# Kernel optimization log

Hardware: AMD Instinct MI355X
Metric: run time of the kernel (lower is better)

The kernel has to match this reference:

```python
import jax, jax.numpy as jnp
import numpy as np

B, T, ENC_H, DEC_H, P = 64, 2048, 512, 512, 256


def setup_inputs() -> dict:
    key = jax.random.key(0)
    ks = jax.random.split(key, 9)
    s_enc = 1.0 / np.sqrt(ENC_H)
    s_dec = 1.0 / np.sqrt(DEC_H)
    return {
        "decoder_output_embedding": jax.random.normal(ks[0], (B, DEC_H), jnp.float32),
        "encoder_outputs": jax.random.normal(ks[1], (B, T, ENC_H), jnp.float32),
        "encoder_lens": jax.random.randint(ks[2], (B,), 1, T + 1, jnp.int64 if jax.config.jax_enable_x64 else jnp.int32),
        # key_proj: Linear(enc_h -> P)
        "Wk": jax.random.uniform(ks[3], (ENC_H, P), jnp.float32, -s_enc, s_enc),
        "bk": jax.random.uniform(ks[4], (P,), jnp.float32, -s_enc, s_enc),
        # encoding_projection (value): Linear(enc_h -> P)
        "Wv": jax.random.uniform(ks[5], (ENC_H, P), jnp.float32, -s_enc, s_enc),
        "bv": jax.random.uniform(ks[6], (P,), jnp.float32, -s_enc, s_enc),
        # query_proj: Linear(dec_h -> P)
        "Wq": jax.random.uniform(ks[7], (DEC_H, P), jnp.float32, -s_dec, s_dec),
        "bq": jax.random.uniform(ks[8], (P,), jnp.float32, -s_dec, s_dec),
    }


def reference(decoder_output_embedding, encoder_outputs, encoder_lens, Wk, bk, Wv, bv, Wq, bq):
    # set_key_value_mask: project encoder outputs to keys and values
    keys = jnp.einsum("bte,ep->btp", encoder_outputs, Wk) + bk      # [B,T,P]
    value = jnp.einsum("bte,ep->btp", encoder_outputs, Wv) + bv     # [B,T,P]
    # forward: project query, score, softmax, weighted sum
    query = decoder_output_embedding @ Wq + bq                        # [B,P]
    raw_weights = jnp.einsum("btp,bp->bt", keys, query)              # [B,T]
    attn = jax.nn.softmax(raw_weights, axis=-1)                       # [B,T]
    context = jnp.einsum("bt,btp->bp", attn, value)                  # [B,P]
    return (context, attn)
```

## Files before the change

### kernel.cpp

```cpp
#include <hip/hip_runtime.h>
#include <math.h>

#define BB 64
#define TT 2048
#define EH 512
#define DH 512
#define PP 256
#define NC 8
#define TC (TT / NC)
#define WPB 8
#define ROWS_PER_WAVE (TC / WPB)

typedef float vfloat4 __attribute__((ext_vector_type(4)));

__global__ __launch_bounds__(256) void k_qproj(
    const float* __restrict__ dec, const float* __restrict__ Wq,
    const float* __restrict__ bq, float* __restrict__ q)
{
    const int b  = blockIdx.x >> 2;
    const int pq = blockIdx.x & 3;
    const int tid = threadIdx.x;
    const int p  = pq * 64 + (tid & 63);
    const int dc = tid >> 6;

    const float* decb = dec + b * DH;
    float a0 = 0.f, a1 = 0.f, a2 = 0.f, a3 = 0.f;
    #pragma unroll 8
    for (int d = dc * 128; d < dc * 128 + 128; d += 4) {
        a0 = fmaf(decb[d + 0], Wq[(d + 0) * PP + p], a0);
        a1 = fmaf(decb[d + 1], Wq[(d + 1) * PP + p], a1);
        a2 = fmaf(decb[d + 2], Wq[(d + 2) * PP + p], a2);
        a3 = fmaf(decb[d + 3], Wq[(d + 3) * PP + p], a3);
    }
    const float acc = (a0 + a1) + (a2 + a3);

    __shared__ float s_red[256];
    s_red[tid] = acc;
    __syncthreads();
    if (tid < 64) {
        float r = s_red[tid] + s_red[tid + 64] + s_red[tid + 128] + s_red[tid + 192];
        q[b * PP + p] = r + bq[p];
    }
}

__global__ __launch_bounds__(256) void k_kfold(
    const float* __restrict__ Wk, const float* __restrict__ q,
    float* __restrict__ qk)
{
    const int b   = blockIdx.x >> 5;
    const int et  = blockIdx.x & 31;
    const int grp = threadIdx.x >> 4;
    const int l16 = threadIdx.x & 15;
    const int e   = et * 16 + grp;

    const float* wrow = Wk + e * PP;
    const float* qb   = q + b * PP;

    float s0 = 0.f, s1 = 0.f, s2 = 0.f, s3 = 0.f;
    #pragma unroll
    for (int k = 0; k < 4; ++k) {
        const float4 w  = *(const float4*)(wrow + l16 * 4 + k * 64);
        const float4 qv = *(const float4*)(qb   + l16 * 4 + k * 64);
        s0 = fmaf(w.x, qv.x, s0);
        s1 = fmaf(w.y, qv.y, s1);
        s2 = fmaf(w.z, qv.z, s2);
        s3 = fmaf(w.w, qv.w, s3);
    }
    float acc = (s0 + s1) + (s2 + s3);
    #pragma unroll
    for (int off = 1; off < 16; off <<= 1)
        acc += __shfl_xor(acc, off, 64);
    if (l16 == 0) qk[b * EH + e] = acc;
}

__global__ __launch_bounds__(512) void attn_main(
    const float* __restrict__ enc,
    const float* __restrict__ qk,
    float* __restrict__ raw,
    float* __restrict__ mc,
    float* __restrict__ lc,
    float* __restrict__ ctxc)
{
    const int blk  = blockIdx.x;
    const int b    = blk >> 3;
    const int c    = blk & (NC - 1);
    const int tid  = threadIdx.x;
    const int wave = tid >> 6;
    const int lane = tid & 63;
    const int e0   = lane * 4;

    const float* encb = enc + (size_t)b * TT * EH;

    const float4 qk0 = *(const float4*)(qk + b * EH + e0);
    const float4 qk1 = *(const float4*)(qk + b * EH + 256 + e0);

    float  m = -1e30f, l = 0.f;
    float4 ctx0 = {0.f, 0.f, 0.f, 0.f};
    float4 ctx1 = {0.f, 0.f, 0.f, 0.f};

    __shared__ float s_raw[TC];
    const int tbase = c * TC + wave;

    const vfloat4* row0 = (const vfloat4*)(encb + (size_t)tbase * EH);
    vfloat4 a0 = __builtin_nontemporal_load(row0 + lane);
    vfloat4 a1 = __builtin_nontemporal_load(row0 + 64 + lane);

    for (int it = 0; it < ROWS_PER_WAVE; ++it) {
        const int itn = (it + 1 < ROWS_PER_WAVE) ? it + 1 : it;
        const vfloat4* nrow = (const vfloat4*)(encb + (size_t)(tbase + WPB * itn) * EH);
        vfloat4 n0 = __builtin_nontemporal_load(nrow + lane);
        vfloat4 n1 = __builtin_nontemporal_load(nrow + 64 + lane);

        float d = a0.x * qk0.x + a0.y * qk0.y + a0.z * qk0.z + a0.w * qk0.w
                + a1.x * qk1.x + a1.y * qk1.y + a1.z * qk1.z + a1.w * qk1.w;
        #pragma unroll
        for (int off = 32; off > 0; off >>= 1)
            d += __shfl_xor(d, off, 64);
        const float s = d;

        if (lane == 0) s_raw[wave + WPB * it] = s;

        const float mn    = fmaxf(m, s);
        const float scale = __expf(m - mn);
        const float p     = __expf(s - mn);
        l = l * scale + p;
        ctx0.x = ctx0.x * scale + p * a0.x;
        ctx0.y = ctx0.y * scale + p * a0.y;
        ctx0.z = ctx0.z * scale + p * a0.z;
        ctx0.w = ctx0.w * scale + p * a0.w;
        ctx1.x = ctx1.x * scale + p * a1.x;
        ctx1.y = ctx1.y * scale + p * a1.y;
        ctx1.z = ctx1.z * scale + p * a1.z;
        ctx1.w = ctx1.w * scale + p * a1.w;
        m = mn;

        a0 = n0; a1 = n1;
    }

    __shared__ float s_m[WPB], s_l[WPB];
    __shared__ float s_ctx[WPB][EH];
    *(float4*)&s_ctx[wave][e0]       = ctx0;
    *(float4*)&s_ctx[wave][256 + e0] = ctx1;
    if (lane == 0) { s_m[wave] = m; s_l[wave] = l; }
    __syncthreads();

    if (tid < TC) raw[(size_t)b * TT + c * TC + tid] = s_raw[tid];

    float mb = s_m[0];
    #pragma unroll
    for (int i = 1; i < WPB; ++i) mb = fmaxf(mb, s_m[i]);
    float w[WPB];
    #pragma unroll
    for (int i = 0; i < WPB; ++i) w[i] = __expf(s_m[i] - mb);

    if (tid == 0) {
        float lsum = 0.f;
        #pragma unroll
        for (int i = 0; i < WPB; ++i) lsum = fmaf(s_l[i], w[i], lsum);
        mc[b * NC + c] = mb;
        lc[b * NC + c] = lsum;
    }
    float accv = 0.f;
    #pragma unroll
    for (int i = 0; i < WPB; ++i) accv = fmaf(s_ctx[i][tid], w[i], accv);
    ctxc[((size_t)b * NC + c) * EH + tid] = accv;
}

__global__ __launch_bounds__(256) void k_finish(
    const float* __restrict__ mc,
    const float* __restrict__ lc,
    const float* __restrict__ ctxc,
    const float* __restrict__ Wv,
    const float* __restrict__ bv,
    float* __restrict__ out_ctx,
    float* __restrict__ attn)
{
    const int b   = blockIdx.x >> 2;
    const int pq  = blockIdx.x & 3;
    const int tid = threadIdx.x;

    float m = -1e30f;
    #pragma unroll
    for (int i = 0; i < NC; ++i) m = fmaxf(m, mc[b * NC + i]);
    float l = 0.f;
    #pragma unroll
    for (int i = 0; i < NC; ++i) l += lc[b * NC + i] * __expf(mc[b * NC + i] - m);
    const float inv_l = 1.0f / l;

    __shared__ float s_w[NC];
    __shared__ float s_ctx[EH];
    if (tid < NC) s_w[tid] = __expf(mc[b * NC + tid] - m);
    __syncthreads();

    for (int e = tid; e < EH; e += 256) {
        float acc = 0.f;
        #pragma unroll
        for (int i = 0; i < NC; ++i)
            acc += ctxc[((size_t)b * NC + i) * EH + e] * s_w[i];
        s_ctx[e] = acc * inv_l;
    }
    __syncthreads();

    const int p  = pq * 64 + (tid & 63);
    const int dc = tid >> 6;
    float a0 = 0.f, a1 = 0.f, a2 = 0.f, a3 = 0.f;
    #pragma unroll 8
    for (int e = dc * 128; e < dc * 128 + 128; e += 4) {
        a0 = fmaf(s_ctx[e + 0], Wv[(e + 0) * PP + p], a0);
        a1 = fmaf(s_ctx[e + 1], Wv[(e + 1) * PP + p], a1);
        a2 = fmaf(s_ctx[e + 2], Wv[(e + 2) * PP + p], a2);
        a3 = fmaf(s_ctx[e + 3], Wv[(e + 3) * PP + p], a3);
    }
    const float acc = (a0 + a1) + (a2 + a3);

    __shared__ float s_red[256];
    s_red[tid] = acc;
    __syncthreads();
    if (tid < 64)
        out_ctx[b * PP + p] = s_red[tid] + s_red[tid + 64]
                            + s_red[tid + 128] + s_red[tid + 192] + bv[p];

    #pragma unroll
    for (int i = 0; i < TT / 4 / 256; ++i) {
        const int t = pq * (TT / 4) + i * 256 + tid;
        const float r = attn[(size_t)b * TT + t];
        attn[(size_t)b * TT + t] = __expf(r - m) * inv_l;
    }
}

extern "C" void kernel_launch(void* const* d_in, const int* in_sizes, int n_in,
                              void* d_out, int out_size, void* d_ws, size_t ws_size,
                              hipStream_t stream) {
    const float* dec = (const float*)d_in[0];
    const float* enc = (const float*)d_in[1];
    const float* Wk  = (const float*)d_in[3];
    const float* Wv  = (const float*)d_in[5];
    const float* bv  = (const float*)d_in[6];
    const float* Wq  = (const float*)d_in[7];
    const float* bq  = (const float*)d_in[8];

    float* out_ctx = (float*)d_out;
    float* attn    = out_ctx + BB * PP;

    float* q    = (float*)d_ws;
    float* qk   = q + BB * PP;
    float* mc   = qk + BB * EH;
    float* lc   = mc + BB * NC;
    float* ctxc = lc + BB * NC;

    k_qproj<<<BB * 4, 256, 0, stream>>>(dec, Wq, bq, q);
    k_kfold<<<BB * 32, 256, 0, stream>>>(Wk, q, qk);
    attn_main<<<BB * NC, 512, 0, stream>>>(enc, qk, attn, mc, lc, ctxc);
    k_finish<<<BB * 4, 256, 0, stream>>>(mc, lc, ctxc, Wv, bv, out_ctx, attn);
}
```

Before: 61.65 us.

## Fuse query/key-fold prep and last-block finish into two kernels

Merges the query projection and the Wk fold into one per-batch prep kernel that keeps q in shared memory, and folds the finish step (chunk merge, Wv projection, attn normalisation) into the main attention kernel. The merge runs in whichever chunk block of a batch increments an atomic counter last. This cuts four launches to two and drops the q workspace round-trip. In exchange, prep uses only 64 blocks that each loop over all of Wk, and the finish work runs serially in a single block per batch.

```diff
diff --git a/kernel.cpp b/kernel.cpp
--- a/kernel.cpp
+++ b/kernel.cpp
@@ -13,73 +13,69 @@
 
 typedef float vfloat4 __attribute__((ext_vector_type(4)));
 
-__global__ __launch_bounds__(256) void k_qproj(
-    const float* __restrict__ dec, const float* __restrict__ Wq,
-    const float* __restrict__ bq, float* __restrict__ q)
+__global__ __launch_bounds__(256) void k_prep(
+    const float* __restrict__ dec,
+    const float* __restrict__ Wq,
+    const float* __restrict__ bq,
+    const float* __restrict__ Wk,
+    float* __restrict__ qk,
+    unsigned int* __restrict__ cnt)
 {
-    const int b  = blockIdx.x >> 2;
-    const int pq = blockIdx.x & 3;
+    const int b   = blockIdx.x;
     const int tid = threadIdx.x;
-    const int p  = pq * 64 + (tid & 63);
-    const int dc = tid >> 6;
-
-    const float* decb = dec + b * DH;
+    if (tid == 0) cnt[b] = 0u;
+
+    __shared__ float s_dec[DH];
+    __shared__ float s_q[PP];
+    for (int d = tid; d < DH; d += 256) s_dec[d] = dec[b * DH + d];
+    __syncthreads();
+
     float a0 = 0.f, a1 = 0.f, a2 = 0.f, a3 = 0.f;
     #pragma unroll 8
-    for (int d = dc * 128; d < dc * 128 + 128; d += 4) {
-        a0 = fmaf(decb[d + 0], Wq[(d + 0) * PP + p], a0);
-        a1 = fmaf(decb[d + 1], Wq[(d + 1) * PP + p], a1);
-        a2 = fmaf(decb[d + 2], Wq[(d + 2) * PP + p], a2);
-        a3 = fmaf(decb[d + 3], Wq[(d + 3) * PP + p], a3);
-    }
-    const float acc = (a0 + a1) + (a2 + a3);
-
-    __shared__ float s_red[256];
-    s_red[tid] = acc;
-    __syncthreads();
-    if (tid < 64) {
-        float r = s_red[tid] + s_red[tid + 64] + s_red[tid + 128] + s_red[tid + 192];
-        q[b * PP + p] = r + bq[p];
+    for (int d = 0; d < DH; d += 4) {
+        a0 = fmaf(s_dec[d + 0], Wq[(d + 0) * PP + tid], a0);
+        a1 = fmaf(s_dec[d + 1], Wq[(d + 1) * PP + tid], a1);
+        a2 = fmaf(s_dec[d + 2], Wq[(d + 2) * PP + tid], a2);
+        a3 = fmaf(s_dec[d + 3], Wq[(d + 3) * PP + tid], a3);
+    }
+    s_q[tid] = (a0 + a1) + (a2 + a3) + bq[tid];
+    __syncthreads();
+
+    const int grp = tid >> 4;
+    const int l16 = tid & 15;
+    #pragma unroll 2
+    for (int r = 0; r < EH / 16; ++r) {
+        const int e = r * 16 + grp;
+        const float* wrow = Wk + (size_t)e * PP;
+        float s0 = 0.f, s1 = 0.f, s2 = 0.f, s3 = 0.f;
+        #pragma unroll
+        for (int k = 0; k < 4; ++k) {
+            const float4 w  = *(const float4*)(wrow + l16 * 4 + k * 64);
+            const float4 qv = *(const float4*)((const float*)s_q + l16 * 4 + k * 64);
+            s0 = fmaf(w.x, qv.x, s0);
+            s1 = fmaf(w.y, qv.y, s1);
+            s2 = fmaf(w.z, qv.z, s2);
+            s3 = fmaf(w.w, qv.w, s3);
+        }
+        float acc = (s0 + s1) + (s2 + s3);
+        #pragma unroll
+        for (int off = 1; off < 16; off <<= 1)
+            acc += __shfl_xor(acc, off, 64);
+        if (l16 == 0) qk[b * EH + e] = acc;
     }
 }
 
-__global__ __launch_bounds__(256) void k_kfold(
-    const float* __restrict__ Wk, const float* __restrict__ q,
-    float* __restrict__ qk)
-{
-    const int b   = blockIdx.x >> 5;
-    const int et  = blockIdx.x & 31;
-    const int grp = threadIdx.x >> 4;
-    const int l16 = threadIdx.x & 15;
-    const int e   = et * 16 + grp;
-
-    const float* wrow = Wk + e * PP;
-    const float* qb   = q + b * PP;
-
-    float s0 = 0.f, s1 = 0.f, s2 = 0.f, s3 = 0.f;
-    #pragma unroll
-    for (int k = 0; k < 4; ++k) {
-        const float4 w  = *(const float4*)(wrow + l16 * 4 + k * 64);
-        const float4 qv = *(const float4*)(qb   + l16 * 4 + k * 64);
-        s0 = fmaf(w.x, qv.x, s0);
-        s1 = fmaf(w.y, qv.y, s1);
-        s2 = fmaf(w.z, qv.z, s2);
-        s3 = fmaf(w.w, qv.w, s3);
-    }
-    float acc = (s0 + s1) + (s2 + s3);
-    #pragma unroll
-    for (int off = 1; off < 16; off <<= 1)
-        acc += __shfl_xor(acc, off, 64);
-    if (l16 == 0) qk[b * EH + e] = acc;
-}
-
-__global__ __launch_bounds__(512) void attn_main(
+__global__ __launch_bounds__(512) void attn_mf(
     const float* __restrict__ enc,
     const float* __restrict__ qk,
-    float* __restrict__ raw,
+    const float* __restrict__ Wv,
+    const float* __restrict__ bv,
+    float* __restrict__ out_ctx,
+    float* __restrict__ attn,
     float* __restrict__ mc,
     float* __restrict__ lc,
-    float* __restrict__ ctxc)
+    float* __restrict__ ctxc,
+    unsigned int* __restrict__ cnt)
 {
     const int blk  = blockIdx.x;
     const int b    = blk >> 3;
@@ -144,7 +140,7 @@
     if (lane == 0) { s_m[wave] = m; s_l[wave] = l; }
     __syncthreads();
 
-    if (tid < TC) raw[(size_t)b * TT + c * TC + tid] = s_raw[tid];
+    if (tid < TC) attn[(size_t)b * TT + c * TC + tid] = s_raw[tid];
 
     float mb = s_m[0];
     #pragma unroll
@@ -164,67 +160,61 @@
     #pragma unroll
     for (int i = 0; i < WPB; ++i) accv = fmaf(s_ctx[i][tid], w[i], accv);
     ctxc[((size_t)b * NC + c) * EH + tid] = accv;
-}
-
-__global__ __launch_bounds__(256) void k_finish(
-    const float* __restrict__ mc,
-    const float* __restrict__ lc,
-    const float* __restrict__ ctxc,
-    const float* __restrict__ Wv,
-    const float* __restrict__ bv,
-    float* __restrict__ out_ctx,
-    float* __restrict__ attn)
-{
-    const int b   = blockIdx.x >> 2;
-    const int pq  = blockIdx.x & 3;
-    const int tid = threadIdx.x;
-
-    float m = -1e30f;
-    #pragma unroll
-    for (int i = 0; i < NC; ++i) m = fmaxf(m, mc[b * NC + i]);
-    float l = 0.f;
-    #pragma unroll
-    for (int i = 0; i < NC; ++i) l += lc[b * NC + i] * __expf(mc[b * NC + i] - m);
-    const float inv_l = 1.0f / l;
-
-    __shared__ float s_w[NC];
-    __shared__ float s_ctx[EH];
-    if (tid < NC) s_w[tid] = __expf(mc[b * NC + tid] - m);
-    __syncthreads();
-
-    for (int e = tid; e < EH; e += 256) {
+
+    __threadfence();
+    __syncthreads();
+    __shared__ unsigned int s_last;
+    if (tid == 0) s_last = (atomicAdd(&cnt[b], 1u) == NC - 1) ? 1u : 0u;
+    __syncthreads();
+    if (s_last == 0u) return;
+    __threadfence();
+
+    float mm = -1e30f;
+    #pragma unroll
+    for (int i = 0; i < NC; ++i) mm = fmaxf(mm, mc[b * NC + i]);
+    float ww[NC];
+    #pragma unroll
+    for (int i = 0; i < NC; ++i) ww[i] = __expf(mc[b * NC + i] - mm);
+    float ll = 0.f;
+    #pragma unroll
+    for (int i = 0; i < NC; ++i) ll = fmaf(lc[b * NC + i], ww[i], ll);
+    const float inv_l = 1.0f / ll;
+
+    __shared__ float s_sctx[EH];
+    {
         float acc = 0.f;
         #pragma unroll
         for (int i = 0; i < NC; ++i)
-            acc += ctxc[((size_t)b * NC + i) * EH + e] * s_w[i];
-        s_ctx[e] = acc * inv_l;
-    }
-    __syncthreads();
-
-    const int p  = pq * 64 + (tid & 63);
-    const int dc = tid >> 6;
-    float a0 = 0.f, a1 = 0.f, a2 = 0.f, a3 = 0.f;
-    #pragma unroll 8
-    for (int e = dc * 128; e < dc * 128 + 128; e += 4) {
-        a0 = fmaf(s_ctx[e + 0], Wv[(e + 0) * PP + p], a0);
-        a1 = fmaf(s_ctx[e + 1], Wv[(e + 1) * PP + p], a1);
-        a2 = fmaf(s_ctx[e + 2], Wv[(e + 2) * PP + p], a2);
-        a3 = fmaf(s_ctx[e + 3], Wv[(e + 3) * PP + p], a3);
-    }
-    const float acc = (a0 + a1) + (a2 + a3);
-
-    __shared__ float s_red[256];
-    s_red[tid] = acc;
-    __syncthreads();
-    if (tid < 64)
-        out_ctx[b * PP + p] = s_red[tid] + s_red[tid + 64]
-                            + s_red[tid + 128] + s_red[tid + 192] + bv[p];
-
-    #pragma unroll
-    for (int i = 0; i < TT / 4 / 256; ++i) {
-        const int t = pq * (TT / 4) + i * 256 + tid;
-        const float r = attn[(size_t)b * TT + t];
-        attn[(size_t)b * TT + t] = __expf(r - m) * inv_l;
+            acc = fmaf(ctxc[((size_t)b * NC + i) * EH + tid], ww[i], acc);
+        s_sctx[tid] = acc * inv_l;
+    }
+    __syncthreads();
+
+    {
+        const int p    = tid & (PP - 1);
+        const int half = tid >> 8;
+        float c0 = 0.f, c1 = 0.f, c2 = 0.f, c3 = 0.f;
+        #pragma unroll 8
+        for (int e = half * 256; e < half * 256 + 256; e += 4) {
+            c0 = fmaf(s_sctx[e + 0], Wv[(e + 0) * PP + p], c0);
+            c1 = fmaf(s_sctx[e + 1], Wv[(e + 1) * PP + p], c1);
+            c2 = fmaf(s_sctx[e + 2], Wv[(e + 2) * PP + p], c2);
+            c3 = fmaf(s_sctx[e + 3], Wv[(e + 3) * PP + p], c3);
+        }
+        __shared__ float s_red[512];
+        s_red[tid] = (c0 + c1) + (c2 + c3);
+        __syncthreads();
+        if (half == 0)
+            out_ctx[b * PP + p] = s_red[tid] + s_red[tid + 256] + bv[p];
+    }
+
+    {
+        float4 r = *(const float4*)(attn + (size_t)b * TT + tid * 4);
+        r.x = __expf(r.x - mm) * inv_l;
+        r.y = __expf(r.y - mm) * inv_l;
+        r.z = __expf(r.z - mm) * inv_l;
+        r.w = __expf(r.w - mm) * inv_l;
+        *(float4*)(attn + (size_t)b * TT + tid * 4) = r;
     }
 }
 
@@ -242,14 +232,13 @@
     float* out_ctx = (float*)d_out;
     float* attn    = out_ctx + BB * PP;
 
-    float* q    = (float*)d_ws;
-    float* qk   = q + BB * PP;
-    float* mc   = qk + BB * EH;
-    float* lc   = mc + BB * NC;
-    float* ctxc = lc + BB * NC;
-
-    k_qproj<<<BB * 4, 256, 0, stream>>>(dec, Wq, bq, q);
-    k_kfold<<<BB * 32, 256, 0, stream>>>(Wk, q, qk);
-    attn_main<<<BB * NC, 512, 0, stream>>>(enc, qk, attn, mc, lc, ctxc);
-    k_finish<<<BB * 4, 256, 0, stream>>>(mc, lc, ctxc, Wv, bv, out_ctx, attn);
+    float* qk          = (float*)d_ws;
+    float* mc          = qk + BB * EH;
+    float* lc          = mc + BB * NC;
+    float* ctxc        = lc + BB * NC;
+    unsigned int* cnt  = (unsigned int*)(ctxc + (size_t)BB * NC * EH);
+
+    k_prep<<<BB, 256, 0, stream>>>(dec, Wq, bq, Wk, qk, cnt);
+    attn_mf<<<BB * NC, 512, 0, stream>>>(enc, qk, Wv, bv, out_ctx, attn,
+                                         mc, lc, ctxc, cnt);
 }
```

After: 206.2 us. +234.4%, slower.

## Fuse query projection and key fold into one kernel; lazy online-softmax rescale

Applied to the files above, without the earlier changes.

Merges the query projection and Wk folding kernels into a single per-batch kernel that keeps q in shared memory, removing one launch and the global round trip for q. The online-softmax loop now rescales the accumulators only when a new maximum appears and uses fmaf updates, cutting exp and multiply work per row. In exchange the prep kernel launches only 64 blocks, each doing serial work over all 512 Wk rows, so it may be latency-bound with low occupancy. The new branch in the main loop is wave-uniform because s is reduced across the wave.

```diff
diff --git a/kernel.cpp b/kernel.cpp
--- a/kernel.cpp
+++ b/kernel.cpp
@@ -13,64 +13,54 @@
 
 typedef float vfloat4 __attribute__((ext_vector_type(4)));
 
-__global__ __launch_bounds__(256) void k_qproj(
-    const float* __restrict__ dec, const float* __restrict__ Wq,
-    const float* __restrict__ bq, float* __restrict__ q)
+__global__ __launch_bounds__(256) void k_prep(
+    const float* __restrict__ dec,
+    const float* __restrict__ Wq,
+    const float* __restrict__ bq,
+    const float* __restrict__ Wk,
+    float* __restrict__ qk)
 {
-    const int b  = blockIdx.x >> 2;
-    const int pq = blockIdx.x & 3;
+    const int b   = blockIdx.x;
     const int tid = threadIdx.x;
-    const int p  = pq * 64 + (tid & 63);
-    const int dc = tid >> 6;
-
-    const float* decb = dec + b * DH;
+
+    __shared__ float s_dec[DH];
+    __shared__ float s_q[PP];
+    for (int d = tid; d < DH; d += 256) s_dec[d] = dec[b * DH + d];
+    __syncthreads();
+
     float a0 = 0.f, a1 = 0.f, a2 = 0.f, a3 = 0.f;
     #pragma unroll 8
-    for (int d = dc * 128; d < dc * 128 + 128; d += 4) {
-        a0 = fmaf(decb[d + 0], Wq[(d + 0) * PP + p], a0);
-        a1 = fmaf(decb[d + 1], Wq[(d + 1) * PP + p], a1);
-        a2 = fmaf(decb[d + 2], Wq[(d + 2) * PP + p], a2);
-        a3 = fmaf(decb[d + 3], Wq[(d + 3) * PP + p], a3);
-    }
-    const float acc = (a0 + a1) + (a2 + a3);
-
-    __shared__ float s_red[256];
-    s_red[tid] = acc;
-    __syncthreads();
-    if (tid < 64) {
-        float r = s_red[tid] + s_red[tid + 64] + s_red[tid + 128] + s_red[tid + 192];
-        q[b * PP + p] = r + bq[p];
-    }
-}
-
-__global__ __launch_bounds__(256) void k_kfold(
-    const float* __restrict__ Wk, const float* __restrict__ q,
-    float* __restrict__ qk)
-{
-    const int b   = blockIdx.x >> 5;
-    const int et  = blockIdx.x & 31;
-    const int grp = threadIdx.x >> 4;
-    const int l16 = threadIdx.x & 15;
-    const int e   = et * 16 + grp;
-
-    const float* wrow = Wk + e * PP;
-    const float* qb   = q + b * PP;
-
-    float s0 = 0.f, s1 = 0.f, s2 = 0.f, s3 = 0.f;
-    #pragma unroll
-    for (int k = 0; k < 4; ++k) {
-        const float4 w  = *(const float4*)(wrow + l16 * 4 + k * 64);
-        const float4 qv = *(const float4*)(qb   + l16 * 4 + k * 64);
-        s0 = fmaf(w.x, qv.x, s0);
-        s1 = fmaf(w.y, qv.y, s1);
-        s2 = fmaf(w.z, qv.z, s2);
-        s3 = fmaf(w.w, qv.w, s3);
-    }
-    float acc = (s0 + s1) + (s2 + s3);
-    #pragma unroll
-    for (int off = 1; off < 16; off <<= 1)
-        acc += __shfl_xor(acc, off, 64);
-    if (l16 == 0) qk[b * EH + e] = acc;
+    for (int d = 0; d < DH; d += 4) {
+        a0 = fmaf(s_dec[d + 0], Wq[(d + 0) * PP + tid], a0);
+        a1 = fmaf(s_dec[d + 1], Wq[(d + 1) * PP + tid], a1);
+        a2 = fmaf(s_dec[d + 2], Wq[(d + 2) * PP + tid], a2);
+        a3 = fmaf(s_dec[d + 3], Wq[(d + 3) * PP + tid], a3);
+    }
+    s_q[tid] = (a0 + a1) + (a2 + a3) + bq[tid];
+    __syncthreads();
+
+    const int grp = tid >> 4;
+    const int l16 = tid & 15;
+    #pragma unroll 2
+    for (int r = 0; r < EH / 16; ++r) {
+        const int e = r * 16 + grp;
+        const float* wrow = Wk + (size_t)e * PP;
+        float s0 = 0.f, s1 = 0.f, s2 = 0.f, s3 = 0.f;
+        #pragma unroll
+        for (int k = 0; k < 4; ++k) {
+            const float4 w  = *(const float4*)(wrow + l16 * 4 + k * 64);
+            const float4 qv = *(const float4*)(s_q + l16 * 4 + k * 64);
+            s0 = fmaf(w.x, qv.x, s0);
+            s1 = fmaf(w.y, qv.y, s1);
+            s2 = fmaf(w.z, qv.z, s2);
+            s3 = fmaf(w.w, qv.w, s3);
+        }
+        float acc = (s0 + s1) + (s2 + s3);
+        #pragma unroll
+        for (int off = 1; off < 16; off <<= 1)
+            acc += __shfl_xor(acc, off, 64);
+        if (l16 == 0) qk[b * EH + e] = acc;
+    }
 }
 
 __global__ __launch_bounds__(512) void attn_main(
@@ -120,19 +110,23 @@
 
         if (lane == 0) s_raw[wave + WPB * it] = s;
 
-        const float mn    = fmaxf(m, s);
-        const float scale = __expf(m - mn);
-        const float p     = __expf(s - mn);
-        l = l * scale + p;
-        ctx0.x = ctx0.x * scale + p * a0.x;
-        ctx0.y = ctx0.y * scale + p * a0.y;
-        ctx0.z = ctx0.z * scale + p * a0.z;
-        ctx0.w = ctx0.w * scale + p * a0.w;
-        ctx1.x = ctx1.x * scale + p * a1.x;
-        ctx1.y = ctx1.y * scale + p * a1.y;
-        ctx1.z = ctx1.z * scale + p * a1.z;
-        ctx1.w = ctx1.w * scale + p * a1.w;
-        m = mn;
+        if (s > m) {
+            const float scale = __expf(m - s);
+            l *= scale;
+            ctx0.x *= scale; ctx0.y *= scale; ctx0.z *= scale; ctx0.w *= scale;
+            ctx1.x *= scale; ctx1.y *= scale; ctx1.z *= scale; ctx1.w *= scale;
+            m = s;
+        }
+        const float p = __expf(s - m);
+        l += p;
+        ctx0.x = fmaf(p, a0.x, ctx0.x);
+        ctx0.y = fmaf(p, a0.y, ctx0.y);
+        ctx0.z = fmaf(p, a0.z, ctx0.z);
+        ctx0.w = fmaf(p, a0.w, ctx0.w);
+        ctx1.x = fmaf(p, a1.x, ctx1.x);
+        ctx1.y = fmaf(p, a1.y, ctx1.y);
+        ctx1.z = fmaf(p, a1.z, ctx1.z);
+        ctx1.w = fmaf(p, a1.w, ctx1.w);
 
         a0 = n0; a1 = n1;
     }
@@ -242,14 +236,12 @@
     float* out_ctx = (float*)d_out;
     float* attn    = out_ctx + BB * PP;
 
-    float* q    = (float*)d_ws;
-    float* qk   = q + BB * PP;
+    float* qk   = (float*)d_ws;
     float* mc   = qk + BB * EH;
     float* lc   = mc + BB * NC;
     float* ctxc = lc + BB * NC;
 
-    k_qproj<<<BB * 4, 256, 0, stream>>>(dec, Wq, bq, q);
-    k_kfold<<<BB * 32, 256, 0, stream>>>(Wk, q, qk);
+    k_prep<<<BB, 256, 0, stream>>>(dec, Wq, bq, Wk, qk);
     attn_main<<<BB * NC, 512, 0, stream>>>(enc, qk, attn, mc, lc, ctxc);
     k_finish<<<BB * 4, 256, 0, stream>>>(mc, lc, ctxc, Wv, bv, out_ctx, attn);
 }
```

After: 67.87 us. +10.1%, slower.
